# Kernel tuning notes

Measured on AMD Instinct MI355X. Metric: run time of the kernel, lower is better.

The kernel has to match this reference:

```python
import jax, jax.numpy as jnp
import numpy as np

B, S, E, D, H, DH, FF, L = 8, 1024, 256, 1024, 16, 64, 4096, 12
TIME_DIM = 4096
MAX_PERIOD = 10000.0


def setup_inputs() -> dict:
    key = jax.random.key(0)
    ks = jax.random.split(key, 12)
    n = lambda k, shp: jax.random.normal(k, shp, dtype=jnp.float32) * 0.02
    return dict(
        inputs=jax.random.normal(ks[0], (B, S, 2 * E), dtype=jnp.float32),
        time=jax.random.uniform(ks[1], (B,), dtype=jnp.float32),
        in_W=n(ks[2], (2 * E, D)), in_b=jnp.zeros((D,), jnp.float32),
        out_W=n(ks[3], (D, E)), out_b=jnp.zeros((E,), jnp.float32),
        t_W1=n(ks[4], (D, TIME_DIM)), t_b1=jnp.zeros((TIME_DIM,), jnp.float32),
        t_W2=n(ks[5], (TIME_DIM, D)), t_b2=jnp.zeros((D,), jnp.float32),
        ln_scale=jnp.ones((L, D), jnp.float32),
        ln_bias=jnp.zeros((L, D), jnp.float32),
        proj_W=n(ks[6], (L, D, 3 * H * DH + 2 * FF)),
        attn_W=n(ks[7], (L, H * DH, D)),
        ff_W=n(ks[8], (L, FF, D)),
    )


def _layernorm(x, g, b):
    m = jnp.mean(x, axis=-1, keepdims=True)
    v = jnp.mean(jnp.square(x - m), axis=-1, keepdims=True)
    return (x - m) * jax.lax.rsqrt(v + 1e-5) * g + b


def reference(inputs, time, in_W, in_b, out_W, out_b, t_W1, t_b1, t_W2, t_b2,
              ln_scale, ln_bias, proj_W, attn_W, ff_W):
    # --- time embedding (SinusoidalTimeEmbedding -> Linear -> GELU -> Linear -> GELU) ---
    half = D // 2
    inv_ts = jnp.exp(jnp.arange(half, dtype=jnp.float32) * (-np.log(MAX_PERIOD) / (half - 1.0)))
    ts = time[:, None] * inv_ts[None, :]                      # [B, D/2]
    temb = jnp.concatenate([jnp.sin(ts), jnp.cos(ts)], -1)     # [B, D]
    temb = jax.nn.gelu(temb @ t_W1 + t_b1, approximate=False)
    temb = jax.nn.gelu(temb @ t_W2 + t_b2, approximate=False)  # [B, D]
    # --- fixed position embedding ---
    inv_freq = 1.0 / (MAX_PERIOD ** (jnp.arange(0, D, 2, dtype=jnp.float32) / D))
    sinu = jnp.arange(S, dtype=jnp.float32)[:, None] * inv_freq[None, :]  # [S, D/2]
    pos = jnp.concatenate([jnp.sin(sinu), jnp.cos(sinu)], -1)             # [S, D]
    # --- input projection + additive embeddings ---
    h = inputs @ in_W + in_b + pos[None] + temb[:, None, :]    # [B, S, D]
    scale = 1.0 / np.sqrt(DH)

    def block(h, params):
        g, bln, Wp, Wa, Wf = params
        u = _layernorm(h, g, bln)
        proj = u @ Wp                                          # [B, S, 3*H*DH + 2*FF]
        q, k, v, ff, gate = jnp.split(
            proj, [H * DH, 2 * H * DH, 3 * H * DH, 3 * H * DH + FF], axis=-1)
        q = q.reshape(B, S, H, DH).transpose(0, 2, 1, 3)       # [B, H, S, DH]
        k = k.reshape(B, S, H, DH).transpose(0, 2, 1, 3)
        v = v.reshape(B, S, H, DH).transpose(0, 2, 1, 3)
        score = jnp.einsum('bhsd,bhtd->bhst', q, k) * scale
        w = jax.nn.softmax(score, axis=-1)
        a = jnp.einsum('bhst,bhtd->bhsd', w, v)
        a = a.transpose(0, 2, 1, 3).reshape(B, S, H * DH)      # merge heads
        attn_out = a @ Wa
        ff_out = (ff * jax.nn.gelu(gate, approximate=True)) @ Wf  # tanh GELU per torch
        return h + attn_out + ff_out, None

    h, _ = jax.lax.scan(block, h, (ln_scale, ln_bias, proj_W, attn_W, ff_W))
    return h @ out_W + out_b
```

## Files before the change

kernel.cpp:

```cpp
#include <hip/hip_runtime.h>
#include <hip/hip_bf16.h>
#include <math.h>

static constexpr int B_ = 8, S_ = 1024, E_ = 256, D_ = 1024, H_ = 16, DH_ = 64,
                     FF_ = 4096, L_ = 12, TDIM_ = 4096;
static constexpr int BS_ = B_ * S_;
static constexpr int PROJN_ = 3 * H_ * DH_ + 2 * FF_;
static constexpr int PROJK_ = 2 * H_ * DH_;
static constexpr int AOW_ = H_ * DH_ + FF_;

typedef __attribute__((ext_vector_type(8))) short bf16x8;
typedef __attribute__((ext_vector_type(4))) short bf16x4;
typedef __attribute__((ext_vector_type(4))) float f32x4;

__device__ __forceinline__ float b2f(short b) {
    return __uint_as_float(((unsigned)(unsigned short)b) << 16);
}
__device__ __forceinline__ short f2b(float f) {
    __hip_bfloat16 h = __float2bfloat16(f);
    return *reinterpret_cast<short*>(&h);
}
__device__ __forceinline__ float gelu_exact(float x) {
    return 0.5f * x * (1.f + erff(x * 0.70710678118654752440f));
}
__device__ __forceinline__ float gelu_tanh(float x) {
    float u2 = 1.59576912160573070f * (x + 0.044715f * x * x * x);
    return x / (1.f + __expf(-u2));
}

#define GLOAD16(g, l)                                                     \
    __builtin_amdgcn_global_load_lds(                                     \
        (const __attribute__((address_space(1))) void*)(g),               \
        (__attribute__((address_space(3))) void*)(l), 16, 0, 0)

__global__ void temb0_kernel(const float* __restrict__ time, float* __restrict__ temb0) {
    int b = blockIdx.x;
    int i = threadIdx.x;
    float inv_ts = expf((float)i * (-logf(10000.f) / 511.f));
    float ts = time[b] * inv_ts;
    temb0[b * D_ + i] = sinf(ts);
    temb0[b * D_ + 512 + i] = cosf(ts);
}

__global__ void pos_kernel(float* __restrict__ pos) {
    int s = blockIdx.x;
    int j = threadIdx.x;
    float inv_freq = expf((float)j * (-logf(10000.f) / 512.f));
    float arg = (float)s * inv_freq;
    pos[s * D_ + j] = sinf(arg);
    pos[s * D_ + 512 + j] = cosf(arg);
}

__global__ void tmlp_kernel(const float* __restrict__ A, const float* __restrict__ Bw,
                            const float* __restrict__ bias, float* __restrict__ C,
                            int K, int N) {
    __shared__ float Ast[8][256];
    __shared__ float red2[16][16][9];
    int t = threadIdx.x;
    int col = t & 15, ks = t >> 4;
    int n = blockIdx.x * 16 + col;
    float acc[8];
#pragma unroll
    for (int b = 0; b < 8; ++b) acc[b] = 0.f;
    for (int c0 = 0; c0 < K; c0 += 256) {
#pragma unroll
        for (int i = 0; i < 8; ++i) {
            int idx = t + i * 256;
            Ast[idx >> 8][idx & 255] = A[(idx >> 8) * K + c0 + (idx & 255)];
        }
        __syncthreads();
#pragma unroll
        for (int i = 0; i < 16; ++i) {
            int k = ks * 16 + i;
            float w = Bw[(size_t)(c0 + k) * N + n];
#pragma unroll
            for (int b = 0; b < 8; ++b) acc[b] = fmaf(Ast[b][k], w, acc[b]);
        }
        __syncthreads();
    }
#pragma unroll
    for (int b = 0; b < 8; ++b) red2[ks][col][b] = acc[b];
    __syncthreads();
    if (t < 128) {
        int c2 = t >> 3, b = t & 7;
        float s = 0.f;
#pragma unroll
        for (int k2 = 0; k2 < 16; ++k2) s += red2[k2][c2][b];
        int nn = blockIdx.x * 16 + c2;
        C[(size_t)b * N + nn] = gelu_exact(s + bias[nn]);
    }
}

__global__ void f2b4_kernel(const float* __restrict__ in, __hip_bfloat16* __restrict__ out) {
    size_t i = ((size_t)blockIdx.x * 256 + threadIdx.x) * 4;
    float4 v = *reinterpret_cast<const float4*>(in + i);
    bf16x4 o;
    o[0] = f2b(v.x); o[1] = f2b(v.y); o[2] = f2b(v.z); o[3] = f2b(v.w);
    *reinterpret_cast<bf16x4*>(reinterpret_cast<short*>(out) + i) = o;
}

__device__ __forceinline__ void convT_body(const float* __restrict__ W,
                                           __hip_bfloat16* __restrict__ Wt,
                                           int K, int N, int outStride, int colOff,
                                           int perm, int bx, int by) {
    __shared__ float tile[64][65];
    int t = threadIdx.x;
    int n0 = bx * 64, k0 = by * 64;
#pragma unroll
    for (int i = 0; i < 4; ++i) {
        int idx = t + i * 256;
        int row = idx >> 4, c4 = (idx & 15) * 4;
        float4 v = *reinterpret_cast<const float4*>(W + (size_t)(k0 + row) * N + n0 + c4);
        tile[row][c4 + 0] = v.x; tile[row][c4 + 1] = v.y;
        tile[row][c4 + 2] = v.z; tile[row][c4 + 3] = v.w;
    }
    __syncthreads();
#pragma unroll
    for (int i = 0; i < 4; ++i) {
        int idx = t + i * 256;
        int n = idx >> 4, k4 = (idx & 15) * 4;
        int ng = n0 + n;
        size_t orow;
        if (perm) {
            if (ng < 3072) orow = ng;
            else if (ng < 7168) { int j = ng - 3072; orow = 3072 + (j >> 7) * 256 + (j & 127); }
            else { int j = ng - 7168; orow = 3072 + (j >> 7) * 256 + 128 + (j & 127); }
        } else {
            orow = ng;
        }
        bf16x4 o;
#pragma unroll
        for (int j = 0; j < 4; ++j) o[j] = f2b(tile[k4 + j][n]);
        *reinterpret_cast<bf16x4*>(reinterpret_cast<short*>(Wt) + orow * outStride + colOff + k0 + k4) = o;
    }
}

__global__ void convT_kernel(const float* __restrict__ W, __hip_bfloat16* __restrict__ Wt,
                             int K, int N, int outStride, int colOff) {
    convT_body(W, Wt, K, N, outStride, colOff, 0, blockIdx.x, blockIdx.y);
}

__global__ void convT3_kernel(const float* __restrict__ Wp, const float* __restrict__ Wa,
                              const float* __restrict__ Wf, __hip_bfloat16* __restrict__ Wpt,
                              __hip_bfloat16* __restrict__ Waft) {
    int bid = blockIdx.x;
    if (bid < 2816) {
        convT_body(Wp, Wpt, D_, PROJN_, D_, 0, 1, bid % 176, bid / 176);
    } else if (bid < 3072) {
        int i2 = bid - 2816;
        convT_body(Wa, Waft, D_, D_, AOW_, 0, 0, i2 & 15, i2 >> 4);
    } else {
        int i2 = bid - 3072;
        convT_body(Wf, Waft, FF_, D_, AOW_, D_, 0, i2 & 15, i2 >> 4);
    }
}

__global__ void ln_kernel(const float* __restrict__ h, const float* __restrict__ g,
                          const float* __restrict__ bb, __hip_bfloat16* __restrict__ u) {
    int row = blockIdx.x;
    int t = threadIdx.x;
    const float4 v = reinterpret_cast<const float4*>(h + (size_t)row * D_)[t];
    __shared__ float red[8];
    float s = v.x + v.y + v.z + v.w;
    for (int m8 = 1; m8 < 64; m8 <<= 1) s += __shfl_xor(s, m8, 64);
    if ((t & 63) == 0) red[t >> 6] = s;
    __syncthreads();
    float mean = (red[0] + red[1] + red[2] + red[3]) * (1.f / 1024.f);
    float dx = v.x - mean, dy = v.y - mean, dz = v.z - mean, dw = v.w - mean;
    float sq = dx * dx + dy * dy + dz * dz + dw * dw;
    for (int m8 = 1; m8 < 64; m8 <<= 1) sq += __shfl_xor(sq, m8, 64);
    if ((t & 63) == 0) red[4 + (t >> 6)] = sq;
    __syncthreads();
    float var = (red[4] + red[5] + red[6] + red[7]) * (1.f / 1024.f);
    float inv = rsqrtf(var + 1e-5f);
    int c = t * 4;
    bf16x4 o;
    o[0] = f2b(dx * inv * g[c + 0] + bb[c + 0]);
    o[1] = f2b(dy * inv * g[c + 1] + bb[c + 1]);
    o[2] = f2b(dz * inv * g[c + 2] + bb[c + 2]);
    o[3] = f2b(dw * inv * g[c + 3] + bb[c + 3]);
    *reinterpret_cast<bf16x4*>(reinterpret_cast<short*>(u) + (size_t)row * D_ + c) = o;
}

template <int MODE, int BIAS, int ADDPE>
__global__ __launch_bounds__(256) void mfma_gemm(
    const __hip_bfloat16* __restrict__ A, const __hip_bfloat16* __restrict__ Bt,
    const float* __restrict__ bias, float* __restrict__ Cf,
    __hip_bfloat16* __restrict__ Cb, const float* __restrict__ pe_pos,
    const float* __restrict__ pe_temb, int M, int N, int K) {
    __shared__ __align__(16) char As[128 * 64];
    __shared__ __align__(16) char Bs[128 * 64];
    int t = threadIdx.x;
    int lane = t & 63, wid = t >> 6;
    int m0 = blockIdx.y * 128, n0 = blockIdx.x * 128;
    size_t rowb = (size_t)K * 2;
    int srow = wid * 32 + (lane >> 2);
    int scol = (lane & 3) * 16;
    const char* ag0 = (const char*)A + (size_t)(m0 + srow) * rowb + scol;
    const char* ag1 = (const char*)A + (size_t)(m0 + srow + 16) * rowb + scol;
    const char* bg0 = (const char*)Bt + (size_t)(n0 + srow) * rowb + scol;
    const char* bg1 = (const char*)Bt + (size_t)(n0 + srow + 16) * rowb + scol;
    int lb0 = wid * 32 * 64;
    int lb1 = lb0 + 16 * 64;
    int wr = (wid >> 1) * 64, wc = (wid & 1) * 64;
    int lr = lane & 15;
    int a_base = (wr + lr) * 64 + (lane >> 4) * 16;
    int b_base = (wc + lr) * 64 + (lane >> 4) * 16;
    f32x4 acc[4][4] = {};
    int nkt = K >> 5;
    for (int kt = 0; kt < nkt; ++kt) {
        GLOAD16(ag0, As + lb0);
        GLOAD16(ag1, As + lb1);
        GLOAD16(bg0, Bs + lb0);
        GLOAD16(bg1, Bs + lb1);
        ag0 += 64; ag1 += 64; bg0 += 64; bg1 += 64;
        __syncthreads();
        bf16x8 af[4], bf[4];
#pragma unroll
        for (int f = 0; f < 4; ++f) {
            af[f] = *reinterpret_cast<const bf16x8*>(As + a_base + f * 1024);
            bf[f] = *reinterpret_cast<const bf16x8*>(Bs + b_base + f * 1024);
        }
        __builtin_amdgcn_s_setprio(1);
#pragma unroll
        for (int i = 0; i < 4; ++i)
#pragma unroll
            for (int j = 0; j < 4; ++j)
                acc[i][j] = __builtin_amdgcn_mfma_f32_16x16x32_bf16(af[i], bf[j], acc[i][j], 0, 0, 0);
        __builtin_amdgcn_s_setprio(0);
        __syncthreads();
    }
    int crow0 = m0 + wr + (lane >> 4) * 4;
    int ccol0 = n0 + wc + lr;
#pragma unroll
    for (int i = 0; i < 4; ++i) {
#pragma unroll
        for (int j = 0; j < 4; ++j) {
            int col = ccol0 + j * 16;
            float bv = BIAS ? bias[col] : 0.f;
            f32x4 v = acc[i][j];
#pragma unroll
            for (int r = 0; r < 4; ++r) {
                int row = crow0 + i * 16 + r;
                size_t o = (size_t)row * N + col;
                float val = v[r] + bv;
                if (ADDPE)
                    val += pe_pos[(size_t)(row & 1023) * D_ + col] +
                           pe_temb[(size_t)(row >> 10) * D_ + col];
                if (MODE == 0) Cf[o] = val;
                else if (MODE == 1) Cb[o] = __float2bfloat16(val);
                else Cf[o] += val;
            }
        }
    }
}

template <int MODE>
__global__ __launch_bounds__(512, 2) void gemm256(
    const __hip_bfloat16* __restrict__ A, const __hip_bfloat16* __restrict__ Bt,
    float* __restrict__ Cf, __hip_bfloat16* __restrict__ Cb,
    __hip_bfloat16* __restrict__ Fb, __hip_bfloat16* __restrict__ Vt,
    int M, int N, int K) {
    __shared__ __align__(16) char lds[131072];
    const int t = threadIdx.x;
    const int lane = t & 63, wid = t >> 6;
    const int lr = lane & 15, g = lane >> 4;
    const int wr = wid >> 2, wc = wid & 3;
    const int nbx = gridDim.x;
    const int nwg = nbx * gridDim.y;
    const int bid = blockIdx.y * nbx + blockIdx.x;
    const int swz = (bid & 7) * (nwg >> 3) + (bid >> 3);
    const int bx = swz % nbx, by = swz / nbx;
    const int m0 = by * 256, n0 = bx * 256;
    const size_t rowb = (size_t)K * 2;
    const int NT = K >> 6;
    const int srow = lane >> 2;
    const int scol = ((lane & 3) ^ (((lane >> 5) & 1) << 1)) * 16;
    const int ga = (g ^ (((lr >> 3) & 1) << 1)) * 16;
    const int arow = wr * 16 + lr;
    const int brow = wc * 16 + lr;
    const char* Ab = (const char*)A;
    const char* Bb = (const char*)Bt;

    auto stage = [&](int mat, int kt, int hh) {
        if (kt >= NT) return;
        int rbase = (mat ? n0 : m0) + hh * 128 + wid * 16 + srow;
        const char* src = (mat ? Bb : Ab) + (size_t)rbase * rowb + (size_t)kt * 128 + scol;
        char* dst = lds + mat * 65536 + (kt & 1) * 32768 + (hh * 128 + wid * 16) * 64;
        GLOAD16(src, dst);
        GLOAD16(src + 64, dst + 16384);
    };

    f32x4 acc[8][4] = {};
    bf16x8 af[4][2], bfr[4][2];

    stage(0, 0, 0); stage(0, 0, 1); stage(1, 0, 0); stage(1, 0, 1);
    stage(0, 1, 0); stage(1, 1, 0); stage(1, 1, 1);
    asm volatile("s_waitcnt vmcnt(6)" ::: "memory");
    __builtin_amdgcn_s_barrier();

    for (int kt = 0; kt < NT; ++kt) {
        const int p = kt & 1;
        const char* la = lds + p * 32768;
        const char* lb = lds + 65536 + p * 32768;
#pragma unroll
        for (int mi = 0; mi < 4; ++mi)
#pragma unroll
            for (int kk = 0; kk < 2; ++kk)
                af[mi][kk] = *reinterpret_cast<const bf16x8*>(
                    la + kk * 16384 + (mi * 32 + arow) * 64 + ga);
#pragma unroll
        for (int n = 0; n < 2; ++n)
#pragma unroll
            for (int kk = 0; kk < 2; ++kk)
                bfr[n][kk] = *reinterpret_cast<const bf16x8*>(
                    lb + kk * 16384 + (n * 64 + brow) * 64 + ga);
        stage(0, kt + 1, 1);
        __builtin_amdgcn_s_barrier();
        asm volatile("s_waitcnt lgkmcnt(0)" ::: "memory");
        __builtin_amdgcn_sched_barrier(0);
        __builtin_amdgcn_s_setprio(1);
#pragma unroll
        for (int mi = 0; mi < 4; ++mi)
#pragma unroll
            for (int n = 0; n < 2; ++n)
#pragma unroll
                for (int kk = 0; kk < 2; ++kk)
                    acc[mi][n] = __builtin_amdgcn_mfma_f32_16x16x32_bf16(
                        af[mi][kk], bfr[n][kk], acc[mi][n], 0, 0, 0);
        __builtin_amdgcn_s_setprio(0);
        __builtin_amdgcn_s_barrier();
#pragma unroll
        for (int n = 2; n < 4; ++n)
#pragma unroll
            for (int kk = 0; kk < 2; ++kk)
                bfr[n][kk] = *reinterpret_cast<const bf16x8*>(
                    lb + kk * 16384 + (n * 64 + brow) * 64 + ga);
        stage(0, kt + 2, 0);
        __builtin_amdgcn_s_barrier();
        asm volatile("s_waitcnt lgkmcnt(0)" ::: "memory");
        __builtin_amdgcn_sched_barrier(0);
        __builtin_amdgcn_s_setprio(1);
#pragma unroll
        for (int mi = 0; mi < 4; ++mi)
#pragma unroll
            for (int n = 2; n < 4; ++n)
#pragma unroll
                for (int kk = 0; kk < 2; ++kk)
                    acc[mi][n] = __builtin_amdgcn_mfma_f32_16x16x32_bf16(
                        af[mi][kk], bfr[n][kk], acc[mi][n], 0, 0, 0);
        __builtin_amdgcn_s_setprio(0);
        __builtin_amdgcn_s_barrier();
#pragma unroll
        for (int mi = 0; mi < 4; ++mi)
#pragma unroll
            for (int kk = 0; kk < 2; ++kk)
                af[mi][kk] = *reinterpret_cast<const bf16x8*>(
                    la + kk * 16384 + ((mi + 4) * 32 + arow) * 64 + ga);
        stage(1, kt + 2, 0);
        __builtin_amdgcn_s_barrier();
        asm volatile("s_waitcnt lgkmcnt(0)" ::: "memory");
        __builtin_amdgcn_sched_barrier(0);
        __builtin_amdgcn_s_setprio(1);
#pragma unroll
        for (int mi = 0; mi < 4; ++mi)
#pragma unroll
            for (int n = 2; n < 4; ++n)
#pragma unroll
                for (int kk = 0; kk < 2; ++kk)
                    acc[mi + 4][n] = __builtin_amdgcn_mfma_f32_16x16x32_bf16(
                        af[mi][kk], bfr[n][kk], acc[mi + 4][n], 0, 0, 0);
        __builtin_amdgcn_s_setprio(0);
        __builtin_amdgcn_s_barrier();
        stage(1, kt + 2, 1);
        if (kt < NT - 2) {
            asm volatile("s_waitcnt vmcnt(6)" ::: "memory");
        } else {
            asm volatile("s_waitcnt vmcnt(0)" ::: "memory");
        }
        __builtin_amdgcn_s_barrier();
        __builtin_amdgcn_s_setprio(1);
#pragma unroll
        for (int mi = 0; mi < 4; ++mi)
#pragma unroll
            for (int n = 0; n < 2; ++n)
#pragma unroll
                for (int kk = 0; kk < 2; ++kk)
                    acc[mi + 4][n] = __builtin_amdgcn_mfma_f32_16x16x32_bf16(
                        af[mi][kk], bfr[n][kk], acc[mi + 4][n], 0, 0, 0);
        __builtin_amdgcn_s_setprio(0);
        __builtin_amdgcn_s_barrier();
    }
    if (MODE == 3 && bx >= 12) {
        int jb = (bx - 12) * 128;
#pragma unroll
        for (int m = 0; m < 8; ++m) {
            int crow = m0 + m * 32 + wr * 16 + g * 4;
#pragma unroll
            for (int n = 0; n < 2; ++n) {
                int ffcol = jb + n * 64 + wc * 16 + lr;
                f32x4 fv = acc[m][n];
                f32x4 gv = acc[m][n + 2];
#pragma unroll
                for (int r = 0; r < 4; ++r) {
                    float val = fv[r] * gelu_tanh(gv[r]);
                    Fb[(size_t)(crow + r) * AOW_ + ffcol] = __float2bfloat16(val);
                }
            }
        }
        return;
    }
    if (MODE == 3 && bx >= 8) {
#pragma unroll
        for (int m = 0; m < 8; ++m) {
            int crow = m0 + m * 32 + wr * 16 + g * 4;
            int b = crow >> 10, s = crow & 1023;
#pragma unroll
            for (int n = 0; n < 4; ++n) {
                int col = n0 + n * 64 + wc * 16 + lr;
                int head = (col - 2048) >> 6, d = col & 63;
                f32x4 v = acc[m][n];
                bf16x4 o;
#pragma unroll
                for (int r = 0; r < 4; ++r) o[r] = f2b(v[r]);
                *reinterpret_cast<bf16x4*>(
                    reinterpret_cast<short*>(Vt) +
                    ((size_t)(b * 16 + head) * 64 + d) * 1024 + s) = o;
            }
        }
        return;
    }
#pragma unroll
    for (int m = 0; m < 8; ++m) {
        int crow = m0 + m * 32 + wr * 16 + g * 4;
#pragma unroll
        for (int n = 0; n < 4; ++n) {
            int col = n0 + n * 64 + wc * 16 + lr;
            f32x4 v = acc[m][n];
#pragma unroll
            for (int r = 0; r < 4; ++r) {
                if (MODE == 3) Cb[(size_t)(crow + r) * PROJK_ + col] = __float2bfloat16(v[r]);
                else if (MODE == 0) Cf[(size_t)(crow + r) * N + col] = v[r];
                else if (MODE == 1) Cb[(size_t)(crow + r) * N + col] = __float2bfloat16(v[r]);
                else Cf[(size_t)(crow + r) * N + col] += v[r];
            }
        }
    }
}

template <int EMITB>
__global__ __launch_bounds__(512, 1) void gemm256b(
    const __hip_bfloat16* __restrict__ A, const __hip_bfloat16* __restrict__ Bt,
    float* __restrict__ Cf, __hip_bfloat16* __restrict__ Cb, int M, int N, int K) {
    __shared__ __align__(16) char lds[98304];
    const int t = threadIdx.x;
    const int lane = t & 63, wid = t >> 6;
    const int lr = lane & 15, g = lane >> 4;
    const int wr = wid >> 1, wc = wid & 1;
    const int nbx = gridDim.x;
    const int nwg = nbx * gridDim.y;
    const int bid = blockIdx.y * nbx + blockIdx.x;
    const int swz = (bid & 7) * (nwg >> 3) + (bid >> 3);
    const int bx = swz % nbx, by = swz / nbx;
    const int m0 = by * 256, n0 = bx * 128;
    const size_t rowb = (size_t)K * 2;
    const int NT = K >> 6;
    const int srow = lane >> 2;
    const int scol = ((lane & 3) ^ (((lane >> 5) & 1) << 1)) * 16;
    const int ga = (g ^ (((lr >> 3) & 1) << 1)) * 16;

    auto stageA = [&](int kt, int hh) {
        if (kt >= NT) return;
        int rowg = hh * 128 + wid * 16 + srow;
        const char* src = (const char*)A + (size_t)(m0 + rowg) * rowb + (size_t)kt * 128 + scol;
        char* dst = lds + (kt & 1) * 32768 + (hh * 128 + wid * 16) * 64;
        GLOAD16(src, dst);
        GLOAD16(src + 64, dst + 16384);
    };
    auto stageB = [&](int kt) {
        if (kt >= NT) return;
        int rowg = wid * 16 + srow;
        const char* src = (const char*)Bt + (size_t)(n0 + rowg) * rowb + (size_t)kt * 128 + scol;
        char* dst = lds + 65536 + (kt & 1) * 16384 + (wid * 16) * 64;
        GLOAD16(src, dst);
        GLOAD16(src + 64, dst + 8192);
    };

    f32x4 acc[4][4] = {};
    bf16x8 af[2][2], bfr[4][2];

    stageA(0, 0); stageA(0, 1); stageB(0);
    stageA(1, 0); stageB(1);
    asm volatile("s_waitcnt vmcnt(4)" ::: "memory");
    __builtin_amdgcn_s_barrier();

    for (int kt = 0; kt < NT; ++kt) {
        const int p = kt & 1;
        const char* la = lds + p * 32768;
        const char* lb = lds + 65536 + p * 16384;
#pragma unroll
        for (int mi = 0; mi < 2; ++mi)
#pragma unroll
            for (int kk = 0; kk < 2; ++kk)
                af[mi][kk] = *reinterpret_cast<const bf16x8*>(
                    la + kk * 16384 + (mi * 64 + wr * 16 + lr) * 64 + ga);
#pragma unroll
        for (int n = 0; n < 2; ++n)
#pragma unroll
            for (int kk = 0; kk < 2; ++kk)
                bfr[n][kk] = *reinterpret_cast<const bf16x8*>(
                    lb + kk * 8192 + (wc * 64 + n * 16 + lr) * 64 + ga);
        stageA(kt + 1, 1);
        __builtin_amdgcn_s_barrier();
        asm volatile("s_waitcnt lgkmcnt(0)" ::: "memory");
        __builtin_amdgcn_sched_barrier(0);
        __builtin_amdgcn_s_setprio(1);
#pragma unroll
        for (int mi = 0; mi < 2; ++mi)
#pragma unroll
            for (int n = 0; n < 2; ++n)
#pragma unroll
                for (int kk = 0; kk < 2; ++kk)
                    acc[mi][n] = __builtin_amdgcn_mfma_f32_16x16x32_bf16(
                        af[mi][kk], bfr[n][kk], acc[mi][n], 0, 0, 0);
        __builtin_amdgcn_s_setprio(0);
        __builtin_amdgcn_s_barrier();
#pragma unroll
        for (int n = 2; n < 4; ++n)
#pragma unroll
            for (int kk = 0; kk < 2; ++kk)
                bfr[n][kk] = *reinterpret_cast<const bf16x8*>(
                    lb + kk * 8192 + (wc * 64 + n * 16 + lr) * 64 + ga);
        stageA(kt + 2, 0);
        __builtin_amdgcn_s_barrier();
        asm volatile("s_waitcnt lgkmcnt(0)" ::: "memory");
        __builtin_amdgcn_sched_barrier(0);
        __builtin_amdgcn_s_setprio(1);
#pragma unroll
        for (int mi = 0; mi < 2; ++mi)
#pragma unroll
            for (int n = 2; n < 4; ++n)
#pragma unroll
                for (int kk = 0; kk < 2; ++kk)
                    acc[mi][n] = __builtin_amdgcn_mfma_f32_16x16x32_bf16(
                        af[mi][kk], bfr[n][kk], acc[mi][n], 0, 0, 0);
        __builtin_amdgcn_s_setprio(0);
        __builtin_amdgcn_s_barrier();
#pragma unroll
        for (int mi = 0; mi < 2; ++mi)
#pragma unroll
            for (int kk = 0; kk < 2; ++kk)
                af[mi][kk] = *reinterpret_cast<const bf16x8*>(
                    la + kk * 16384 + ((mi + 2) * 64 + wr * 16 + lr) * 64 + ga);
        stageB(kt + 2);
        __builtin_amdgcn_s_barrier();
        asm volatile("s_waitcnt lgkmcnt(0)" ::: "memory");
        __builtin_amdgcn_sched_barrier(0);
        __builtin_amdgcn_s_setprio(1);
#pragma unroll
        for (int mi = 0; mi < 2; ++mi)
#pragma unroll
            for (int n = 2; n < 4; ++n)
#pragma unroll
                for (int kk = 0; kk < 2; ++kk)
                    acc[mi + 2][n] = __builtin_amdgcn_mfma_f32_16x16x32_bf16(
                        af[mi][kk], bfr[n][kk], acc[mi + 2][n], 0, 0, 0);
        __builtin_amdgcn_s_setprio(0);
        __builtin_amdgcn_s_barrier();
        if (kt < NT - 2) {
            asm volatile("s_waitcnt vmcnt(4)" ::: "memory");
        } else {
            asm volatile("s_waitcnt vmcnt(0)" ::: "memory");
        }
        __builtin_amdgcn_s_barrier();
        __builtin_amdgcn_s_setprio(1);
#pragma unroll
        for (int mi = 0; mi < 2; ++mi)
#pragma unroll
            for (int n = 0; n < 2; ++n)
#pragma unroll
                for (int kk = 0; kk < 2; ++kk)
                    acc[mi + 2][n] = __builtin_amdgcn_mfma_f32_16x16x32_bf16(
                        af[mi][kk], bfr[n][kk], acc[mi + 2][n], 0, 0, 0);
        __builtin_amdgcn_s_setprio(0);
        __builtin_amdgcn_s_barrier();
    }
#pragma unroll
    for (int mq = 0; mq < 4; ++mq) {
        int crow = m0 + mq * 64 + wr * 16 + g * 4;
#pragma unroll
        for (int nq = 0; nq < 4; ++nq) {
            int col = n0 + wc * 64 + nq * 16 + lr;
            f32x4 v = acc[mq][nq];
#pragma unroll
            for (int r = 0; r < 4; ++r) {
                size_t o = (size_t)(crow + r) * N + col;
                float nv = Cf[o] + v[r];
                Cf[o] = nv;
                if (EMITB) Cb[o] = __float2bfloat16(nv);
            }
        }
    }
}

__global__ __launch_bounds__(256, 2) void attn_kernel(
    const __hip_bfloat16* __restrict__ proj, const __hip_bfloat16* __restrict__ vt,
    __hip_bfloat16* __restrict__ ao) {
    __shared__ __align__(16) char ksm[64 * 128];
    __shared__ __align__(16) char vsm[64 * 128];
    __shared__ __align__(16) char psm[4 * 16 * 128];
    int wgid = blockIdx.x;
    int xcd = wgid & 7, slot = wgid >> 3;
    int group = xcd * 16 + (slot >> 4);
    int qt = slot & 15;
    int head = group & 15, b = group >> 4;
    int t = threadIdx.x;
    int lane = t & 63, w = t >> 6;
    int r = lane & 15, g = lane >> 4;
    int r7s = (r & 7) << 4;
    int q0 = qt * 64;
    int qcol = head * 64;
    const __hip_bfloat16* pb = proj + (size_t)b * S_ * PROJK_;
    const char* vtb = (const char*)(vt + ((size_t)(b * 16 + head) * 64) * 1024);
    bf16x8 qf[2];
#pragma unroll
    for (int kk = 0; kk < 2; ++kk)
        qf[kk] = *reinterpret_cast<const bf16x8*>(
            pb + (size_t)(q0 + w * 16 + r) * PROJK_ + qcol + kk * 32 + g * 8);
    int srow8 = lane >> 3;
    int sgrp = lane & 7;
    float m = -1e30f, l = 0.f;
    f32x4 o_acc[4] = {};
    char* pw = psm + w * 2048;
    for (int kt = 0; kt < 16; ++kt) {
        int k0 = kt * 64;
#pragma unroll
        for (int c = 0; c < 2; ++c) {
            int krow = w * 16 + c * 8 + srow8;
            const __hip_bfloat16* src =
                pb + (size_t)(k0 + krow) * PROJK_ + 1024 + qcol + ((sgrp ^ (krow & 7)) << 3);
            GLOAD16(src, ksm + (w * 16 + c * 8) * 128);
        }
#pragma unroll
        for (int c = 0; c < 2; ++c) {
            int drow = w * 16 + c * 8 + srow8;
            const char* src = vtb + (size_t)drow * 2048 + k0 * 2 + ((sgrp ^ (drow & 7)) << 4);
            GLOAD16(src, vsm + (w * 16 + c * 8) * 128);
        }
        __syncthreads();
        f32x4 st[4] = {};
        __builtin_amdgcn_s_setprio(1);
#pragma unroll
        for (int j = 0; j < 4; ++j) {
#pragma unroll
            for (int kk = 0; kk < 2; ++kk) {
                bf16x8 kf = *reinterpret_cast<const bf16x8*>(
                    ksm + (j * 16 + r) * 128 + ((((kk * 4 + g) << 4) ^ r7s)));
                st[j] = __builtin_amdgcn_mfma_f32_16x16x32_bf16(kf, qf[kk], st[j], 0, 0, 0);
            }
        }
        __builtin_amdgcn_s_setprio(0);
        float tmax = -1e30f;
#pragma unroll
        for (int j = 0; j < 4; ++j)
#pragma unroll
            for (int rr = 0; rr < 4; ++rr) {
                st[j][rr] *= 0.125f;
                tmax = fmaxf(tmax, st[j][rr]);
            }
        tmax = fmaxf(tmax, __shfl_xor(tmax, 16, 64));
        tmax = fmaxf(tmax, __shfl_xor(tmax, 32, 64));
        float mnew = fmaxf(m, tmax);
        float rsum = 0.f;
#pragma unroll
        for (int j = 0; j < 4; ++j)
#pragma unroll
            for (int rr = 0; rr < 4; ++rr) {
                float p = __expf(st[j][rr] - mnew);
                st[j][rr] = p;
                rsum += p;
            }
        rsum += __shfl_xor(rsum, 16, 64);
        rsum += __shfl_xor(rsum, 32, 64);
        float alpha = __expf(m - mnew);
        l = l * alpha + rsum;
        m = mnew;
#pragma unroll
        for (int j = 0; j < 4; ++j)
#pragma unroll
            for (int rr = 0; rr < 4; ++rr) {
                int kv2 = j * 32 + g * 8 + rr * 2;
                *reinterpret_cast<short*>(pw + r * 128 + (kv2 ^ r7s)) = f2b(st[j][rr]);
            }
        asm volatile("s_waitcnt lgkmcnt(0)" ::: "memory");
        __builtin_amdgcn_sched_barrier(0);
        float ar[4];
#pragma unroll
        for (int rr = 0; rr < 4; ++rr) ar[rr] = __shfl(alpha, g * 4 + rr, 64);
#pragma unroll
        for (int dt = 0; dt < 4; ++dt)
#pragma unroll
            for (int rr = 0; rr < 4; ++rr) o_acc[dt][rr] *= ar[rr];
        __builtin_amdgcn_s_setprio(1);
#pragma unroll
        for (int kk = 0; kk < 2; ++kk) {
            bf16x8 pf = *reinterpret_cast<const bf16x8*>(
                pw + r * 128 + ((((kk * 4 + g) << 4) ^ r7s)));
#pragma unroll
            for (int dt = 0; dt < 4; ++dt) {
                bf16x8 vf = *reinterpret_cast<const bf16x8*>(
                    vsm + (dt * 16 + r) * 128 + ((((kk * 4 + g) << 4) ^ r7s)));
                o_acc[dt] = __builtin_amdgcn_mfma_f32_16x16x32_bf16(pf, vf, o_acc[dt], 0, 0, 0);
            }
        }
        __builtin_amdgcn_s_setprio(0);
        __syncthreads();
    }
    float linv = 1.f / l;
    float lr4[4];
#pragma unroll
    for (int rr = 0; rr < 4; ++rr) lr4[rr] = __shfl(linv, g * 4 + rr, 64);
    short* ap = reinterpret_cast<short*>(ao);
#pragma unroll
    for (int dt = 0; dt < 4; ++dt)
#pragma unroll
        for (int rr = 0; rr < 4; ++rr) {
            size_t o = ((size_t)b * S_ + q0 + w * 16 + g * 4 + rr) * (size_t)AOW_ +
                       qcol + dt * 16 + r;
            ap[o] = f2b(o_acc[dt][rr] * lr4[rr]);
        }
}

extern "C" void kernel_launch(void* const* d_in, const int* in_sizes, int n_in,
                              void* d_out, int out_size, void* d_ws, size_t ws_size,
                              hipStream_t stream) {
    const float* inputs = (const float*)d_in[0];
    const float* time = (const float*)d_in[1];
    const float* in_W = (const float*)d_in[2];
    const float* in_b = (const float*)d_in[3];
    const float* out_W = (const float*)d_in[4];
    const float* out_b = (const float*)d_in[5];
    const float* t_W1 = (const float*)d_in[6];
    const float* t_b1 = (const float*)d_in[7];
    const float* t_W2 = (const float*)d_in[8];
    const float* t_b2 = (const float*)d_in[9];
    const float* ln_scale = (const float*)d_in[10];
    const float* ln_bias = (const float*)d_in[11];
    const float* proj_W = (const float*)d_in[12];
    const float* attn_W = (const float*)d_in[13];
    const float* ff_W = (const float*)d_in[14];
    float* out = (float*)d_out;

    float* ws = (float*)d_ws;
    size_t off = 0;
    float* temb0 = ws + off; off += 8 * 1024;
    float* tact = ws + off;  off += 8 * 4096;
    float* temb = ws + off;  off += 8 * 1024;
    float* pos = ws + off;   off += (size_t)S_ * D_;
    float* h = ws + off;     off += (size_t)BS_ * D_;
    __hip_bfloat16* u = (__hip_bfloat16*)(ws + off);      off += (size_t)BS_ * D_ / 2;
    __hip_bfloat16* proj = (__hip_bfloat16*)(ws + off);   off += (size_t)BS_ * PROJK_ / 2;
    __hip_bfloat16* vt = (__hip_bfloat16*)(ws + off);     off += (size_t)BS_ * D_ / 2;
    __hip_bfloat16* ao = (__hip_bfloat16*)(ws + off);     off += (size_t)BS_ * AOW_ / 2;
    __hip_bfloat16* hb = (__hip_bfloat16*)(ws + off);     off += (size_t)BS_ * D_ / 2;
    __hip_bfloat16* inbf = (__hip_bfloat16*)(ws + off);   off += (size_t)BS_ * (2 * E_) / 2;
    __hip_bfloat16* in_Wt = (__hip_bfloat16*)(ws + off);  off += (size_t)(2 * E_) * D_ / 2;
    __hip_bfloat16* out_Wt = (__hip_bfloat16*)(ws + off); off += (size_t)D_ * E_ / 2;
    __hip_bfloat16* Wpt = (__hip_bfloat16*)(ws + off);    off += (size_t)D_ * PROJN_ / 2;
    __hip_bfloat16* Waft = (__hip_bfloat16*)(ws + off);   off += (size_t)D_ * AOW_ / 2;

    dim3 blk(256);

    temb0_kernel<<<B_, 512, 0, stream>>>(time, temb0);
    tmlp_kernel<<<TDIM_ / 16, blk, 0, stream>>>(temb0, t_W1, t_b1, tact, D_, TDIM_);
    tmlp_kernel<<<D_ / 16, blk, 0, stream>>>(tact, t_W2, t_b2, temb, TDIM_, D_);
    pos_kernel<<<S_, 512, 0, stream>>>(pos);
    f2b4_kernel<<<(BS_ * 2 * E_) / 1024, blk, 0, stream>>>(inputs, inbf);
    convT_kernel<<<dim3(D_ / 64, (2 * E_) / 64), blk, 0, stream>>>(
        in_W, in_Wt, 2 * E_, D_, 2 * E_, 0);
    convT_kernel<<<dim3(E_ / 64, D_ / 64), blk, 0, stream>>>(
        out_W, out_Wt, D_, E_, D_, 0);
    mfma_gemm<0, 1, 1><<<dim3(D_ / 128, BS_ / 128), blk, 0, stream>>>(
        inbf, in_Wt, in_b, h, nullptr, pos, temb, BS_, D_, 2 * E_);

    for (int l = 0; l < L_; ++l) {
        const float* Wp = proj_W + (size_t)l * D_ * PROJN_;
        const float* Wa = attn_W + (size_t)l * (H_ * DH_) * D_;
        const float* Wf = ff_W + (size_t)l * FF_ * D_;
        convT3_kernel<<<dim3(4096), blk, 0, stream>>>(Wp, Wa, Wf, Wpt, Waft);
        ln_kernel<<<BS_, blk, 0, stream>>>(h, ln_scale + l * D_, ln_bias + l * D_, u);
        gemm256<3><<<dim3(PROJN_ / 256, BS_ / 256), dim3(512), 0, stream>>>(
            u, Wpt, nullptr, proj, ao + D_, vt, BS_, PROJN_, D_);
        attn_kernel<<<dim3(2048), blk, 0, stream>>>(proj, vt, ao);
        if (l == L_ - 1)
            gemm256b<1><<<dim3(D_ / 128, BS_ / 256), dim3(512), 0, stream>>>(
                ao, Waft, h, hb, BS_, D_, AOW_);
        else
            gemm256b<0><<<dim3(D_ / 128, BS_ / 256), dim3(512), 0, stream>>>(
                ao, Waft, h, nullptr, BS_, D_, AOW_);
    }
    mfma_gemm<0, 1, 0><<<dim3(E_ / 128, BS_ / 128), blk, 0, stream>>>(
        hb, out_Wt, out_b, out, nullptr, nullptr, nullptr, BS_, E_, D_);
}
```

Measured before the change: 4.891 ms.

## Double-buffer K/V in attention with 8-wave blocks and fuse layernorm with weight conversion

```diff
diff --git a/kernel.cpp b/kernel.cpp
--- a/kernel.cpp
+++ b/kernel.cpp
@@ -140,24 +140,10 @@
     convT_body(W, Wt, K, N, outStride, colOff, 0, blockIdx.x, blockIdx.y);
 }
 
-__global__ void convT3_kernel(const float* __restrict__ Wp, const float* __restrict__ Wa,
-                              const float* __restrict__ Wf, __hip_bfloat16* __restrict__ Wpt,
-                              __hip_bfloat16* __restrict__ Waft) {
-    int bid = blockIdx.x;
-    if (bid < 2816) {
-        convT_body(Wp, Wpt, D_, PROJN_, D_, 0, 1, bid % 176, bid / 176);
-    } else if (bid < 3072) {
-        int i2 = bid - 2816;
-        convT_body(Wa, Waft, D_, D_, AOW_, 0, 0, i2 & 15, i2 >> 4);
-    } else {
-        int i2 = bid - 3072;
-        convT_body(Wf, Waft, FF_, D_, AOW_, D_, 0, i2 & 15, i2 >> 4);
-    }
-}
-
-__global__ void ln_kernel(const float* __restrict__ h, const float* __restrict__ g,
-                          const float* __restrict__ bb, __hip_bfloat16* __restrict__ u) {
-    int row = blockIdx.x;
+__device__ __forceinline__ void ln_body(const float* __restrict__ h,
+                                        const float* __restrict__ g,
+                                        const float* __restrict__ bb,
+                                        __hip_bfloat16* __restrict__ u, int row) {
     int t = threadIdx.x;
     const float4 v = reinterpret_cast<const float4*>(h + (size_t)row * D_)[t];
     __shared__ float red[8];
@@ -180,6 +166,28 @@
     o[2] = f2b(dz * inv * g[c + 2] + bb[c + 2]);
     o[3] = f2b(dw * inv * g[c + 3] + bb[c + 3]);
     *reinterpret_cast<bf16x4*>(reinterpret_cast<short*>(u) + (size_t)row * D_ + c) = o;
+}
+
+__global__ void prep_kernel(const float* __restrict__ h, const float* __restrict__ g,
+                            const float* __restrict__ bb, __hip_bfloat16* __restrict__ u,
+                            const float* __restrict__ Wp, const float* __restrict__ Wa,
+                            const float* __restrict__ Wf, __hip_bfloat16* __restrict__ Wpt,
+                            __hip_bfloat16* __restrict__ Waft) {
+    int bid = blockIdx.x;
+    if (bid < BS_) {
+        ln_body(h, g, bb, u, bid);
+        return;
+    }
+    int cid = bid - BS_;
+    if (cid < 2816) {
+        convT_body(Wp, Wpt, D_, PROJN_, D_, 0, 1, cid % 176, cid / 176);
+    } else if (cid < 3072) {
+        int i2 = cid - 2816;
+        convT_body(Wa, Waft, D_, D_, AOW_, 0, 0, i2 & 15, i2 >> 4);
+    } else {
+        int i2 = cid - 3072;
+        convT_body(Wf, Waft, FF_, D_, AOW_, D_, 0, i2 & 15, i2 >> 4);
+    }
 }
 
 template <int MODE, int BIAS, int ADDPE>
@@ -603,22 +611,22 @@
     }
 }
 
-__global__ __launch_bounds__(256, 2) void attn_kernel(
+__global__ __launch_bounds__(512, 4) void attn_kernel(
     const __hip_bfloat16* __restrict__ proj, const __hip_bfloat16* __restrict__ vt,
     __hip_bfloat16* __restrict__ ao) {
-    __shared__ __align__(16) char ksm[64 * 128];
-    __shared__ __align__(16) char vsm[64 * 128];
-    __shared__ __align__(16) char psm[4 * 16 * 128];
+    __shared__ __align__(16) char ksm[2][64 * 128];
+    __shared__ __align__(16) char vsm[2][64 * 128];
+    __shared__ __align__(16) char psm[8 * 16 * 128];
     int wgid = blockIdx.x;
     int xcd = wgid & 7, slot = wgid >> 3;
-    int group = xcd * 16 + (slot >> 4);
-    int qt = slot & 15;
+    int group = xcd * 16 + (slot >> 3);
+    int qt = slot & 7;
     int head = group & 15, b = group >> 4;
     int t = threadIdx.x;
     int lane = t & 63, w = t >> 6;
     int r = lane & 15, g = lane >> 4;
     int r7s = (r & 7) << 4;
-    int q0 = qt * 64;
+    int q0 = qt * 128;
     int qcol = head * 64;
     const __hip_bfloat16* pb = proj + (size_t)b * S_ * PROJK_;
     const char* vtb = (const char*)(vt + ((size_t)(b * 16 + head) * 64) * 1024);
@@ -629,25 +637,28 @@
             pb + (size_t)(q0 + w * 16 + r) * PROJK_ + qcol + kk * 32 + g * 8);
     int srow8 = lane >> 3;
     int sgrp = lane & 7;
+    auto stageKV = [&](int ktile) {
+        int k0 = ktile * 64, nb = ktile & 1;
+        int krow = w * 8 + srow8;
+        const __hip_bfloat16* src =
+            pb + (size_t)(k0 + krow) * PROJK_ + 1024 + qcol + ((sgrp ^ (krow & 7)) << 3);
+        GLOAD16(src, ksm[nb] + w * 8 * 128);
+        const char* vsrc = vtb + (size_t)krow * 2048 + k0 * 2 + ((sgrp ^ (krow & 7)) << 4);
+        GLOAD16(vsrc, vsm[nb] + w * 8 * 128);
+    };
     float m = -1e30f, l = 0.f;
     f32x4 o_acc[4] = {};
     char* pw = psm + w * 2048;
+    stageKV(0);
     for (int kt = 0; kt < 16; ++kt) {
-        int k0 = kt * 64;
-#pragma unroll
-        for (int c = 0; c < 2; ++c) {
-            int krow = w * 16 + c * 8 + srow8;
-            const __hip_bfloat16* src =
-                pb + (size_t)(k0 + krow) * PROJK_ + 1024 + qcol + ((sgrp ^ (krow & 7)) << 3);
-            GLOAD16(src, ksm + (w * 16 + c * 8) * 128);
-        }
-#pragma unroll
-        for (int c = 0; c < 2; ++c) {
-            int drow = w * 16 + c * 8 + srow8;
-            const char* src = vtb + (size_t)drow * 2048 + k0 * 2 + ((sgrp ^ (drow & 7)) << 4);
-            GLOAD16(src, vsm + (w * 16 + c * 8) * 128);
-        }
-        __syncthreads();
+        const int cb = kt & 1;
+        if (kt < 15) {
+            stageKV(kt + 1);
+            asm volatile("s_waitcnt vmcnt(2)" ::: "memory");
+        } else {
+            asm volatile("s_waitcnt vmcnt(0)" ::: "memory");
+        }
+        __builtin_amdgcn_s_barrier();
         f32x4 st[4] = {};
         __builtin_amdgcn_s_setprio(1);
 #pragma unroll
@@ -655,7 +666,7 @@
 #pragma unroll
             for (int kk = 0; kk < 2; ++kk) {
                 bf16x8 kf = *reinterpret_cast<const bf16x8*>(
-                    ksm + (j * 16 + r) * 128 + ((((kk * 4 + g) << 4) ^ r7s)));
+                    ksm[cb] + (j * 16 + r) * 128 + ((((kk * 4 + g) << 4) ^ r7s)));
                 st[j] = __builtin_amdgcn_mfma_f32_16x16x32_bf16(kf, qf[kk], st[j], 0, 0, 0);
             }
         }
@@ -709,12 +720,12 @@
 #pragma unroll
             for (int dt = 0; dt < 4; ++dt) {
                 bf16x8 vf = *reinterpret_cast<const bf16x8*>(
-                    vsm + (dt * 16 + r) * 128 + ((((kk * 4 + g) << 4) ^ r7s)));
+                    vsm[cb] + (dt * 16 + r) * 128 + ((((kk * 4 + g) << 4) ^ r7s)));
                 o_acc[dt] = __builtin_amdgcn_mfma_f32_16x16x32_bf16(pf, vf, o_acc[dt], 0, 0, 0);
             }
         }
         __builtin_amdgcn_s_setprio(0);
-        __syncthreads();
+        __builtin_amdgcn_s_barrier();
     }
     float linv = 1.f / l;
     float lr4[4];
@@ -787,11 +798,11 @@
         const float* Wp = proj_W + (size_t)l * D_ * PROJN_;
         const float* Wa = attn_W + (size_t)l * (H_ * DH_) * D_;
         const float* Wf = ff_W + (size_t)l * FF_ * D_;
-        convT3_kernel<<<dim3(4096), blk, 0, stream>>>(Wp, Wa, Wf, Wpt, Waft);
-        ln_kernel<<<BS_, blk, 0, stream>>>(h, ln_scale + l * D_, ln_bias + l * D_, u);
+        prep_kernel<<<dim3(BS_ + 4096), blk, 0, stream>>>(
+            h, ln_scale + l * D_, ln_bias + l * D_, u, Wp, Wa, Wf, Wpt, Waft);
         gemm256<3><<<dim3(PROJN_ / 256, BS_ / 256), dim3(512), 0, stream>>>(
             u, Wpt, nullptr, proj, ao + D_, vt, BS_, PROJN_, D_);
-        attn_kernel<<<dim3(2048), blk, 0, stream>>>(proj, vt, ao);
+        attn_kernel<<<dim3(1024), dim3(512), 0, stream>>>(proj, vt, ao);
         if (l == L_ - 1)
             gemm256b<1><<<dim3(D_ / 128, BS_ / 256), dim3(512), 0, stream>>>(
                 ao, Waft, h, hb, BS_, D_, AOW_);
```

New measurement: 4.932 ms. No clear change (+0.8%).
